# Kernel optimization log

Measured on AMD Instinct MI355X. Metric: run time of the kernel, lower is better.

## Reference

```python
import jax, jax.numpy as jnp
import numpy as np

D_MODEL = 1024
N_HEADS = 16
HEAD_DIM = D_MODEL // N_HEADS
B, S = 2, 2048


def setup_inputs() -> dict:
    key = jax.random.key(0)
    ks = jax.random.split(key, 12)
    std = 1.0 / np.sqrt(D_MODEL)
    mk = lambda k: (jax.random.normal(k, (D_MODEL, D_MODEL), jnp.float32) * std)
    return {
        "query": jax.random.normal(ks[0], (B, S, D_MODEL), jnp.float32),
        "key": jax.random.normal(ks[1], (B, S, D_MODEL), jnp.float32),
        "value": jax.random.normal(ks[2], (B, S, D_MODEL), jnp.float32),
        "Wq": mk(ks[3]), "bq": jnp.zeros((D_MODEL,), jnp.float32),
        "Wk": mk(ks[4]), "bk": jnp.zeros((D_MODEL,), jnp.float32),
        "Wv": mk(ks[5]), "bv": jnp.zeros((D_MODEL,), jnp.float32),
        "Wo": mk(ks[6]), "bo": jnp.zeros((D_MODEL,), jnp.float32),
    }


def reference(query, key, value, Wq, bq, Wk, bk, Wv, bv, Wo, bo):
    b, s, d = query.shape
    # Linear projections (torch Linear: x @ W.T + b)
    q = query @ Wq.T + bq
    k = key @ Wk.T + bk
    v = value @ Wv.T + bv
    # [B, H, S, Dh]
    split = lambda x: x.reshape(b, -1, N_HEADS, HEAD_DIM).transpose(0, 2, 1, 3)
    qh, kh, vh = split(q), split(k), split(v)
    scores = jnp.einsum("bhqd,bhkd->bhqk", qh, kh) / jnp.sqrt(
        jnp.asarray(HEAD_DIM, qh.dtype))
    attn = jax.nn.softmax(scores, axis=-1)
    out = jnp.einsum("bhqk,bhkd->bhqd", attn, vh)
    out = out.transpose(0, 2, 1, 3).reshape(b, -1, N_HEADS * HEAD_DIM)
    return out @ Wo.T + bo
```

## Files before the change

kernel.cpp:

```cpp
#include <hip/hip_runtime.h>
#include <hip/hip_bf16.h>


typedef short bf16x8 __attribute__((ext_vector_type(8)));
typedef short bf16x4 __attribute__((ext_vector_type(4)));
typedef float f32x4  __attribute__((ext_vector_type(4)));

constexpr size_t NE = (size_t)4096 * 1024;
constexpr size_t NW = (size_t)1024 * 1024;

#if __has_builtin(__builtin_amdgcn_exp2f)
#define EXP2(x) __builtin_amdgcn_exp2f(x)
#else
#define EXP2(x) exp2f(x)
#endif

__device__ __forceinline__ short f2bf(float f) {
  __hip_bfloat16 h = __float2bfloat16(f);
  return *reinterpret_cast<short*>(&h);
}

__device__ __forceinline__ void cp16(const short* g, short* l) {
  __builtin_amdgcn_global_load_lds(
      (const __attribute__((address_space(1))) void*)g,
      (__attribute__((address_space(3))) void*)l, 16, 0, 0);
}

__device__ __forceinline__ int xcd_swz(int x, int nblk) {
  return (x & 7) * (nblk >> 3) + (x >> 3);
}

__global__ __launch_bounds__(256) void cvt_kernel(
    const float* q, const float* k, const float* v,
    const float* Wq, const float* Wk, const float* Wv, const float* Wo,
    short* qb, short* kb, short* vb,
    short* Wqb, short* Wkb, short* Wvb, short* Wob) {
  const int y = blockIdx.y;
  const float* s; short* d;
  if (y < 12) {
    const int t = y >> 2;
    const size_t off = (size_t)(y & 3) << 20;
    s = (t == 0 ? q : (t == 1 ? k : v)) + off;
    d = (t == 0 ? qb : (t == 1 ? kb : vb)) + off;
  } else {
    s = (y == 12 ? Wq : (y == 13 ? Wk : (y == 14 ? Wv : Wo)));
    d = (y == 12 ? Wqb : (y == 13 ? Wkb : (y == 14 ? Wvb : Wob)));
  }
  size_t i = (size_t)blockIdx.x * 256 + threadIdx.x;
  float4 val = ((const float4*)s)[i];
  bf16x4 o;
  o[0] = f2bf(val.x); o[1] = f2bf(val.y); o[2] = f2bf(val.z); o[3] = f2bf(val.w);
  ((bf16x4*)d)[i] = o;
}

__global__ __launch_bounds__(256) void gemm_qkv(
    const short* __restrict__ A0, const short* __restrict__ A1, const short* __restrict__ A2,
    const short* __restrict__ W0, const short* __restrict__ W1, const short* __restrict__ W2,
    const float* __restrict__ b0, const float* __restrict__ b1, const float* __restrict__ b2,
    short* __restrict__ C0, short* __restrict__ C1, short* __restrict__ Cv) {
  __shared__ short As[3][128 * 32];
  __shared__ short Bs[3][128 * 32];
  const int which = blockIdx.y;
  const short* A    = which == 0 ? A0 : (which == 1 ? A1 : A2);
  const short* W    = which == 0 ? W0 : (which == 1 ? W1 : W2);
  const float* bias = which == 0 ? b0 : (which == 1 ? b1 : b2);
  const float scale = which == 0 ? 0.18033688011112042f : 1.0f;

  const int tid  = threadIdx.x;
  const int bx   = xcd_swz((int)blockIdx.x, 256);
  const int bm   = bx >> 3;
  const int bn   = bx & 7;
  const int lane = tid & 63, wid = tid >> 6;
  const int g = lane >> 4, l15 = lane & 15;
  const int wm = (wid >> 1) * 64, wn = (wid & 1) * 64;

  const short* Ag = A + (size_t)(bm * 128 + (tid >> 2)) * 1024 + (tid & 3) * 8;
  const short* Wg = W + (size_t)(bn * 128 + (tid >> 2)) * 1024 + (tid & 3) * 8;
  const int wofs = wid * 512;

#define QKV_STAGE(t, b)                               \
  do {                                                \
    const int kk_ = (t) * 32;                         \
    cp16(Ag + kk_,             As[(b)] + wofs);       \
    cp16(Ag + 64 * 1024 + kk_, As[(b)] + wofs + 2048);\
    cp16(Wg + kk_,             Bs[(b)] + wofs);       \
    cp16(Wg + 64 * 1024 + kk_, Bs[(b)] + wofs + 2048);\
  } while (0)

  f32x4 acc[4][4];
#pragma unroll
  for (int i = 0; i < 4; ++i)
#pragma unroll
    for (int j = 0; j < 4; ++j) acc[i][j] = (f32x4){0.f, 0.f, 0.f, 0.f};

  QKV_STAGE(0, 0);
  QKV_STAGE(1, 1);

  for (int t = 0; t < 32; ++t) {
    const int cur = t % 3;
    if (t < 30) {
      QKV_STAGE(t + 2, (t + 2) % 3);
      asm volatile("s_waitcnt vmcnt(8)" ::: "memory");
    } else if (t == 30) {
      asm volatile("s_waitcnt vmcnt(4)" ::: "memory");
    } else {
      asm volatile("s_waitcnt vmcnt(0)" ::: "memory");
    }
    __builtin_amdgcn_s_barrier();

    bf16x8 af[4], bfr[4];
#pragma unroll
    for (int mt = 0; mt < 4; ++mt)
      af[mt] = *(const bf16x8*)&As[cur][(wm + mt * 16 + l15) * 32 + g * 8];
#pragma unroll
    for (int nt = 0; nt < 4; ++nt)
      bfr[nt] = *(const bf16x8*)&Bs[cur][(wn + nt * 16 + l15) * 32 + g * 8];
#pragma unroll
    for (int mt = 0; mt < 4; ++mt)
#pragma unroll
      for (int nt = 0; nt < 4; ++nt)
        acc[mt][nt] = __builtin_amdgcn_mfma_f32_16x16x32_bf16(
            af[mt], bfr[nt], acc[mt][nt], 0, 0, 0);

    asm volatile("s_waitcnt lgkmcnt(0)" ::: "memory");
    __builtin_amdgcn_s_barrier();
  }
#undef QKV_STAGE

  const int col0 = bn * 128 + wn;
  if (which < 2) {
    short* C = which == 0 ? C0 : C1;
#pragma unroll
    for (int nt = 0; nt < 4; ++nt) {
      const int col = col0 + nt * 16 + l15;
      const float bb = bias[col];
#pragma unroll
      for (int mt = 0; mt < 4; ++mt) {
        const int m0 = bm * 128 + wm + mt * 16 + g * 4;
#pragma unroll
        for (int r = 0; r < 4; ++r)
          C[(size_t)(m0 + r) * 1024 + col] = f2bf((acc[mt][nt][r] + bb) * scale);
      }
    }
  } else {
#pragma unroll
    for (int nt = 0; nt < 4; ++nt) {
      const int col = col0 + nt * 16 + l15;
      const int h = col >> 6, dh = col & 63;
      const float bb = bias[col];
#pragma unroll
      for (int mt = 0; mt < 4; ++mt) {
        const int m0 = bm * 128 + wm + mt * 16 + g * 4;
        const int bb_ = m0 >> 11, s0 = m0 & 2047;
        const int k6 = s0 & 63;
        const int cpos = (s0 & ~63) | (((k6 >> 4) & 2) << 4)
                       | (((k6 >> 2) & 3) << 3) | (((k6 >> 4) & 1) << 2);
        bf16x4 o;
#pragma unroll
        for (int r = 0; r < 4; ++r) o[r] = f2bf(acc[mt][nt][r] + bb);
        *(bf16x4*)&Cv[(((size_t)bb_ * 16 + h) * 64 + dh) * 2048 + cpos] = o;
      }
    }
  }
}

__global__ __launch_bounds__(256) void gemm_out(
    const short* __restrict__ A, const short* __restrict__ W,
    const float* __restrict__ bias, float* __restrict__ C) {
  __shared__ short As[3][64 * 32];
  __shared__ short Bs[3][128 * 32];
  const int tid  = threadIdx.x;
  const int bx   = xcd_swz((int)blockIdx.x, 512);
  const int bm   = bx >> 3;
  const int bn   = bx & 7;
  const int lane = tid & 63, wid = tid >> 6;
  const int g = lane >> 4, l15 = lane & 15;
  const int wm = (wid >> 1) * 32, wn = (wid & 1) * 64;

  const short* Ag = A + (size_t)(bm * 64 + (tid >> 2)) * 1024 + (tid & 3) * 8;
  const short* Wg = W + (size_t)(bn * 128 + (tid >> 2)) * 1024 + (tid & 3) * 8;
  const int wofs = wid * 512;

#define OUT_STAGE(t, b)                               \
  do {                                                \
    const int kk_ = (t) * 32;                         \
    cp16(Ag + kk_,             As[(b)] + wofs);       \
    cp16(Wg + kk_,             Bs[(b)] + wofs);       \
    cp16(Wg + 64 * 1024 + kk_, Bs[(b)] + wofs + 2048);\
  } while (0)

  f32x4 acc[2][4];
#pragma unroll
  for (int i = 0; i < 2; ++i)
#pragma unroll
    for (int j = 0; j < 4; ++j) acc[i][j] = (f32x4){0.f, 0.f, 0.f, 0.f};

  OUT_STAGE(0, 0);
  OUT_STAGE(1, 1);

  for (int t = 0; t < 32; ++t) {
    const int cur = t % 3;
    if (t < 30) {
      OUT_STAGE(t + 2, (t + 2) % 3);
      asm volatile("s_waitcnt vmcnt(6)" ::: "memory");
    } else if (t == 30) {
      asm volatile("s_waitcnt vmcnt(3)" ::: "memory");
    } else {
      asm volatile("s_waitcnt vmcnt(0)" ::: "memory");
    }
    __builtin_amdgcn_s_barrier();

    bf16x8 af[2], bfr[4];
#pragma unroll
    for (int mt = 0; mt < 2; ++mt)
      af[mt] = *(const bf16x8*)&As[cur][(wm + mt * 16 + l15) * 32 + g * 8];
#pragma unroll
    for (int nt = 0; nt < 4; ++nt)
      bfr[nt] = *(const bf16x8*)&Bs[cur][(wn + nt * 16 + l15) * 32 + g * 8];
#pragma unroll
    for (int mt = 0; mt < 2; ++mt)
#pragma unroll
      for (int nt = 0; nt < 4; ++nt)
        acc[mt][nt] = __builtin_amdgcn_mfma_f32_16x16x32_bf16(
            af[mt], bfr[nt], acc[mt][nt], 0, 0, 0);

    asm volatile("s_waitcnt lgkmcnt(0)" ::: "memory");
    __builtin_amdgcn_s_barrier();
  }
#undef OUT_STAGE

  const int col0 = bn * 128 + wn;
#pragma unroll
  for (int nt = 0; nt < 4; ++nt) {
    const int col = col0 + nt * 16 + l15;
    const float bb = bias[col];
#pragma unroll
    for (int mt = 0; mt < 2; ++mt) {
      const int m0 = bm * 64 + wm + mt * 16 + g * 4;
#pragma unroll
      for (int r = 0; r < 4; ++r)
        C[(size_t)(m0 + r) * 1024 + col] = acc[mt][nt][r] + bb;
    }
  }
}

__global__ __launch_bounds__(512, 4) void attn_kernel(
    const short* __restrict__ Q, const short* __restrict__ K,
    const short* __restrict__ Vg, short* __restrict__ O) {
  __shared__ __align__(16) char smem[36864];
  short (*Kt)[64][72] = (short(*)[64][72])smem;
  short (*Vt)[64][72] = (short(*)[64][72])(smem + 18432);
  float* M = (float*)smem;

  const int tid  = threadIdx.x;
  const int bx   = xcd_swz((int)blockIdx.x, 512);
  const int qt   = bx & 15;
  const int bh   = bx >> 4;
  const int b    = bh >> 4, h = bh & 15;
  const int lane = tid & 63, wid = tid >> 6;
  const int par  = wid >> 2;
  const int w4   = wid & 3;
  const int g = lane >> 4, l15 = lane & 15;

  const int q0 = qt * 128 + w4 * 32;
  bf16x8 qf[2][2];
#pragma unroll
  for (int mt = 0; mt < 2; ++mt) {
    const size_t base = (size_t)(b * 2048 + q0 + mt * 16 + l15) * 1024 + h * 64;
    qf[mt][0] = *(const bf16x8*)(Q + base + g * 8);
    qf[mt][1] = *(const bf16x8*)(Q + base + 32 + g * 8);
  }

  f32x4 o_acc[2][4];
#pragma unroll
  for (int i = 0; i < 2; ++i)
#pragma unroll
    for (int j = 0; j < 4; ++j) o_acc[i][j] = (f32x4){0.f, 0.f, 0.f, 0.f};
  float l_i[2] = {0.f, 0.f};

  const int st   = tid & 255;
  const int spar = tid >> 8;
  const int srow = st >> 2, sch = st & 3;
  const short* Kbase = K + (size_t)(b * 2048) * 1024 + h * 64 + sch * 8;
  const short* Vbase = Vg + (size_t)((b * 16 + h) * 64 + srow) * 2048 + sch * 8;

  bf16x8 nk0, nk1, nv0, nv1;
  {
    const short* krow = Kbase + (size_t)(spar * 64 + srow) * 1024;
    nk0 = *(const bf16x8*)(krow);
    nk1 = *(const bf16x8*)(krow + 32);
    nv0 = *(const bf16x8*)(Vbase + spar * 64);
    nv1 = *(const bf16x8*)(Vbase + spar * 64 + 32);
  }

  for (int ktp = 0; ktp < 16; ++ktp) {
    __syncthreads();
    *(bf16x8*)&Kt[spar][srow][sch * 8]      = nk0;
    *(bf16x8*)&Kt[spar][srow][sch * 8 + 32] = nk1;
    *(bf16x8*)&Vt[spar][srow][sch * 8]      = nv0;
    *(bf16x8*)&Vt[spar][srow][sch * 8 + 32] = nv1;
    __syncthreads();

    if (ktp < 15) {
      const int kn = (ktp + 1) * 2 + spar;
      const short* krow = Kbase + (size_t)(kn * 64 + srow) * 1024;
      nk0 = *(const bf16x8*)(krow);
      nk1 = *(const bf16x8*)(krow + 32);
      nv0 = *(const bf16x8*)(Vbase + kn * 64);
      nv1 = *(const bf16x8*)(Vbase + kn * 64 + 32);
    }

    f32x4 sv[2][4];
#pragma unroll
    for (int nt = 0; nt < 4; ++nt) {
      bf16x8 kf0 = *(const bf16x8*)&Kt[par][nt * 16 + l15][g * 8];
      bf16x8 kf1 = *(const bf16x8*)&Kt[par][nt * 16 + l15][32 + g * 8];
#pragma unroll
      for (int mt = 0; mt < 2; ++mt) {
        f32x4 z = (f32x4){0.f, 0.f, 0.f, 0.f};
        z = __builtin_amdgcn_mfma_f32_16x16x32_bf16(kf0, qf[mt][0], z, 0, 0, 0);
        z = __builtin_amdgcn_mfma_f32_16x16x32_bf16(kf1, qf[mt][1], z, 0, 0, 0);
        sv[mt][nt] = z;
      }
    }

    bf16x8 pf[2][2];
#pragma unroll
    for (int mt = 0; mt < 2; ++mt) {
      float s = 0.f;
#pragma unroll
      for (int nt = 0; nt < 4; ++nt)
#pragma unroll
        for (int r = 0; r < 4; ++r) {
          float p = EXP2(sv[mt][nt][r]);
          s += p;
          pf[mt][nt >> 1][(nt & 1) * 4 + r] = f2bf(p);
        }
      l_i[mt] += s;
    }

#pragma unroll
    for (int nt = 0; nt < 4; ++nt) {
      bf16x8 vf0 = *(const bf16x8*)&Vt[par][nt * 16 + l15][g * 8];
      bf16x8 vf1 = *(const bf16x8*)&Vt[par][nt * 16 + l15][32 + g * 8];
#pragma unroll
      for (int mt = 0; mt < 2; ++mt) {
        o_acc[mt][nt] = __builtin_amdgcn_mfma_f32_16x16x32_bf16(
            vf0, pf[mt][0], o_acc[mt][nt], 0, 0, 0);
        o_acc[mt][nt] = __builtin_amdgcn_mfma_f32_16x16x32_bf16(
            vf1, pf[mt][1], o_acc[mt][nt], 0, 0, 0);
      }
    }
  }

  __syncthreads();
  if (par == 1) {
    float* dst = M + (size_t)(w4 * 64 + lane) * 36;
#pragma unroll
    for (int mt = 0; mt < 2; ++mt)
#pragma unroll
      for (int nt = 0; nt < 4; ++nt)
        *(f32x4*)(dst + (mt * 4 + nt) * 4) = o_acc[mt][nt];
    dst[32] = l_i[0];
    dst[33] = l_i[1];
  }
  __syncthreads();
  if (par == 0) {
    const float* src = M + (size_t)(w4 * 64 + lane) * 36;
#pragma unroll
    for (int mt = 0; mt < 2; ++mt)
#pragma unroll
      for (int nt = 0; nt < 4; ++nt)
        o_acc[mt][nt] += *(const f32x4*)(src + (mt * 4 + nt) * 4);
    l_i[0] += src[32];
    l_i[1] += src[33];

#pragma unroll
    for (int mt = 0; mt < 2; ++mt) {
      float l = l_i[mt];
      l += __shfl_xor(l, 16, 64);
      l += __shfl_xor(l, 32, 64);
      const float inv = 1.0f / l;
      const int row = q0 + mt * 16 + l15;
      const size_t base = (size_t)(b * 2048 + row) * 1024 + h * 64;
#pragma unroll
      for (int nt = 0; nt < 4; ++nt) {
        bf16x4 o;
#pragma unroll
        for (int r = 0; r < 4; ++r) o[r] = f2bf(o_acc[mt][nt][r] * inv);
        *(bf16x4*)&O[base + nt * 16 + g * 4] = o;
      }
    }
  }
}

extern "C" void kernel_launch(void* const* d_in, const int* in_sizes, int n_in,
                              void* d_out, int out_size, void* d_ws, size_t ws_size,
                              hipStream_t stream) {
  (void)in_sizes; (void)n_in; (void)out_size; (void)ws_size;
  const float* q  = (const float*)d_in[0];
  const float* k  = (const float*)d_in[1];
  const float* v  = (const float*)d_in[2];
  const float* Wq = (const float*)d_in[3];
  const float* bq = (const float*)d_in[4];
  const float* Wk = (const float*)d_in[5];
  const float* bk = (const float*)d_in[6];
  const float* Wv = (const float*)d_in[7];
  const float* bv = (const float*)d_in[8];
  const float* Wo = (const float*)d_in[9];
  const float* bo = (const float*)d_in[10];
  float* out = (float*)d_out;

  short* qb  = (short*)d_ws;
  short* kb  = qb + NE;
  short* vb  = kb + NE;
  short* Wqb = vb + NE;
  short* Wkb = Wqb + NW;
  short* Wvb = Wkb + NW;
  short* Wob = Wvb + NW;
  short* Qw  = Wob + NW;
  short* Kw  = Qw + NE;
  short* Vtg = Kw + NE;
  short* Ob  = qb;

  cvt_kernel<<<dim3(1024, 16), 256, 0, stream>>>(q, k, v, Wq, Wk, Wv, Wo,
                                                 qb, kb, vb, Wqb, Wkb, Wvb, Wob);
  gemm_qkv<<<dim3(256, 3), 256, 0, stream>>>(qb, kb, vb, Wqb, Wkb, Wvb,
                                             bq, bk, bv, Qw, Kw, Vtg);
  attn_kernel<<<512, 512, 0, stream>>>(Qw, Kw, Vtg, Ob);
  gemm_out<<<512, 256, 0, stream>>>(Ob, Wob, bo, out);
}
```

Before: 211.2 us.

## Restructure attention to 4 waves with async double-buffered LDS loads and XOR swizzle

The attention kernel drops the two-way key split across 8 waves in favor of 4 waves, each walking all 32 key tiles. K and V tiles move straight from global memory to LDS with global_load_lds into double buffers, using vmcnt waits and raw barriers, and an XOR swizzle replaces the padded layout to avoid bank conflicts. This removes the register round-trip staging and the final cross-wave reduction through LDS. In exchange each block does a longer serial loop with half the threads, so there is less parallelism per CU.

```diff
diff --git a/kernel.cpp b/kernel.cpp
--- a/kernel.cpp
+++ b/kernel.cpp
@@ -244,13 +244,11 @@
   }
 }
 
-__global__ __launch_bounds__(512, 4) void attn_kernel(
+__global__ __launch_bounds__(256, 4) void attn_kernel(
     const short* __restrict__ Q, const short* __restrict__ K,
     const short* __restrict__ Vg, short* __restrict__ O) {
-  __shared__ __align__(16) char smem[36864];
-  short (*Kt)[64][72] = (short(*)[64][72])smem;
-  short (*Vt)[64][72] = (short(*)[64][72])(smem + 18432);
-  float* M = (float*)smem;
+  __shared__ __align__(16) short KT[2][64 * 64];
+  __shared__ __align__(16) short VT[2][64 * 64];
 
   const int tid  = threadIdx.x;
   const int bx   = xcd_swz((int)blockIdx.x, 512);
@@ -258,11 +256,10 @@
   const int bh   = bx >> 4;
   const int b    = bh >> 4, h = bh & 15;
   const int lane = tid & 63, wid = tid >> 6;
-  const int par  = wid >> 2;
-  const int w4   = wid & 3;
   const int g = lane >> 4, l15 = lane & 15;
-
-  const int q0 = qt * 128 + w4 * 32;
+  const int sx = l15 & 7;
+
+  const int q0 = qt * 128 + wid * 32;
   bf16x8 qf[2][2];
 #pragma unroll
   for (int mt = 0; mt < 2; ++mt) {
@@ -278,43 +275,38 @@
     for (int j = 0; j < 4; ++j) o_acc[i][j] = (f32x4){0.f, 0.f, 0.f, 0.f};
   float l_i[2] = {0.f, 0.f};
 
-  const int st   = tid & 255;
-  const int spar = tid >> 8;
-  const int srow = st >> 2, sch = st & 3;
-  const short* Kbase = K + (size_t)(b * 2048) * 1024 + h * 64 + sch * 8;
-  const short* Vbase = Vg + (size_t)((b * 16 + h) * 64 + srow) * 2048 + sch * 8;
-
-  bf16x8 nk0, nk1, nv0, nv1;
-  {
-    const short* krow = Kbase + (size_t)(spar * 64 + srow) * 1024;
-    nk0 = *(const bf16x8*)(krow);
-    nk1 = *(const bf16x8*)(krow + 32);
-    nv0 = *(const bf16x8*)(Vbase + spar * 64);
-    nv1 = *(const bf16x8*)(Vbase + spar * 64 + 32);
-  }
-
-  for (int ktp = 0; ktp < 16; ++ktp) {
-    __syncthreads();
-    *(bf16x8*)&Kt[spar][srow][sch * 8]      = nk0;
-    *(bf16x8*)&Kt[spar][srow][sch * 8 + 32] = nk1;
-    *(bf16x8*)&Vt[spar][srow][sch * 8]      = nv0;
-    *(bf16x8*)&Vt[spar][srow][sch * 8 + 32] = nv1;
-    __syncthreads();
-
-    if (ktp < 15) {
-      const int kn = (ktp + 1) * 2 + spar;
-      const short* krow = Kbase + (size_t)(kn * 64 + srow) * 1024;
-      nk0 = *(const bf16x8*)(krow);
-      nk1 = *(const bf16x8*)(krow + 32);
-      nv0 = *(const bf16x8*)(Vbase + kn * 64);
-      nv1 = *(const bf16x8*)(Vbase + kn * 64 + 32);
-    }
+  const int lrow = lane >> 3;
+  const int qc   = (lane & 7) ^ lrow;
+  const int r0   = wid * 16;
+  const short* KgA = K + (size_t)(b * 2048 + r0 + lrow) * 1024 + h * 64 + qc * 8;
+  const short* VgA = Vg + (size_t)((b * 16 + h) * 64 + r0 + lrow) * 2048 + qc * 8;
+
+#define ATTN_STAGE(kt_, bf_)                                                 \
+  do {                                                                       \
+    cp16(KgA + (size_t)(kt_) * 64 * 1024,       &KT[bf_][r0 * 64]);          \
+    cp16(KgA + (size_t)((kt_) * 64 + 8) * 1024, &KT[bf_][(r0 + 8) * 64]);    \
+    cp16(VgA + (kt_) * 64,                      &VT[bf_][r0 * 64]);          \
+    cp16(VgA + (kt_) * 64 + 8 * 2048,           &VT[bf_][(r0 + 8) * 64]);    \
+  } while (0)
+
+  ATTN_STAGE(0, 0);
+
+  for (int kt = 0; kt < 32; ++kt) {
+    const int cur = kt & 1;
+    if (kt < 31) {
+      ATTN_STAGE(kt + 1, cur ^ 1);
+      asm volatile("s_waitcnt vmcnt(4)" ::: "memory");
+    } else {
+      asm volatile("s_waitcnt vmcnt(0)" ::: "memory");
+    }
+    __builtin_amdgcn_s_barrier();
 
     f32x4 sv[2][4];
 #pragma unroll
     for (int nt = 0; nt < 4; ++nt) {
-      bf16x8 kf0 = *(const bf16x8*)&Kt[par][nt * 16 + l15][g * 8];
-      bf16x8 kf1 = *(const bf16x8*)&Kt[par][nt * 16 + l15][32 + g * 8];
+      const int krow = (nt * 16 + l15) * 64;
+      bf16x8 kf0 = *(const bf16x8*)&KT[cur][krow + ((g ^ sx) << 3)];
+      bf16x8 kf1 = *(const bf16x8*)&KT[cur][krow + (((g + 4) ^ sx) << 3)];
 #pragma unroll
       for (int mt = 0; mt < 2; ++mt) {
         f32x4 z = (f32x4){0.f, 0.f, 0.f, 0.f};
@@ -341,8 +333,9 @@
 
 #pragma unroll
     for (int nt = 0; nt < 4; ++nt) {
-      bf16x8 vf0 = *(const bf16x8*)&Vt[par][nt * 16 + l15][g * 8];
-      bf16x8 vf1 = *(const bf16x8*)&Vt[par][nt * 16 + l15][32 + g * 8];
+      const int vrow = (nt * 16 + l15) * 64;
+      bf16x8 vf0 = *(const bf16x8*)&VT[cur][vrow + ((g ^ sx) << 3)];
+      bf16x8 vf1 = *(const bf16x8*)&VT[cur][vrow + (((g + 4) ^ sx) << 3)];
 #pragma unroll
       for (int mt = 0; mt < 2; ++mt) {
         o_acc[mt][nt] = __builtin_amdgcn_mfma_f32_16x16x32_bf16(
@@ -351,45 +344,26 @@
             vf1, pf[mt][1], o_acc[mt][nt], 0, 0, 0);
       }
     }
-  }
-
-  __syncthreads();
-  if (par == 1) {
-    float* dst = M + (size_t)(w4 * 64 + lane) * 36;
-#pragma unroll
-    for (int mt = 0; mt < 2; ++mt)
-#pragma unroll
-      for (int nt = 0; nt < 4; ++nt)
-        *(f32x4*)(dst + (mt * 4 + nt) * 4) = o_acc[mt][nt];
-    dst[32] = l_i[0];
-    dst[33] = l_i[1];
-  }
-  __syncthreads();
-  if (par == 0) {
-    const float* src = M + (size_t)(w4 * 64 + lane) * 36;
-#pragma unroll
-    for (int mt = 0; mt < 2; ++mt)
-#pragma unroll
-      for (int nt = 0; nt < 4; ++nt)
-        o_acc[mt][nt] += *(const f32x4*)(src + (mt * 4 + nt) * 4);
-    l_i[0] += src[32];
-    l_i[1] += src[33];
-
-#pragma unroll
-    for (int mt = 0; mt < 2; ++mt) {
-      float l = l_i[mt];
-      l += __shfl_xor(l, 16, 64);
-      l += __shfl_xor(l, 32, 64);
-      const float inv = 1.0f / l;
-      const int row = q0 + mt * 16 + l15;
-      const size_t base = (size_t)(b * 2048 + row) * 1024 + h * 64;
-#pragma unroll
-      for (int nt = 0; nt < 4; ++nt) {
-        bf16x4 o;
-#pragma unroll
-        for (int r = 0; r < 4; ++r) o[r] = f2bf(o_acc[mt][nt][r] * inv);
-        *(bf16x4*)&O[base + nt * 16 + g * 4] = o;
-      }
+
+    asm volatile("s_waitcnt lgkmcnt(0)" ::: "memory");
+    __builtin_amdgcn_s_barrier();
+  }
+#undef ATTN_STAGE
+
+#pragma unroll
+  for (int mt = 0; mt < 2; ++mt) {
+    float l = l_i[mt];
+    l += __shfl_xor(l, 16, 64);
+    l += __shfl_xor(l, 32, 64);
+    const float inv = 1.0f / l;
+    const int row = q0 + mt * 16 + l15;
+    const size_t base = (size_t)(b * 2048 + row) * 1024 + h * 64;
+#pragma unroll
+    for (int nt = 0; nt < 4; ++nt) {
+      bf16x4 o;
+#pragma unroll
+      for (int r = 0; r < 4; ++r) o[r] = f2bf(o_acc[mt][nt][r] * inv);
+      *(bf16x4*)&O[base + nt * 16 + g * 4] = o;
     }
   }
 }
@@ -427,6 +401,6 @@
                                                  qb, kb, vb, Wqb, Wkb, Wvb, Wob);
   gemm_qkv<<<dim3(256, 3), 256, 0, stream>>>(qb, kb, vb, Wqb, Wkb, Wvb,
                                              bq, bk, bv, Qw, Kw, Vtg);
-  attn_kernel<<<512, 512, 0, stream>>>(Qw, Kw, Vtg, Ob);
+  attn_kernel<<<512, 256, 0, stream>>>(Qw, Kw, Vtg, Ob);
   gemm_out<<<512, 256, 0, stream>>>(Ob, Wob, bo, out);
 }
```

Result: no change. 208.1 us (-1.5%).
